# Optimization experiments

Measured on AMD Instinct MI355X. Metric: run time of the kernel, lower is better.

Reference implementation:

```python
import jax, jax.numpy as jnp
import numpy as np

BOUND = 10.0
EPS = 1e-06
MIN_SCALE = 1e-4


def _params_to_spline(raw_w, raw_h, raw_s, bound):
    # Standard Durkan et al. rational-quadratic spline parameterization.
    # raw_w/raw_h: (1, D, K); raw_s: (1, D, K+1)
    two_b = 2.0 * bound
    widths = jax.nn.softmax(raw_w[0], axis=-1) * two_b      # (D, K)
    heights = jax.nn.softmax(raw_h[0], axis=-1) * two_b     # (D, K)
    zero = jnp.zeros(widths.shape[:-1] + (1,), widths.dtype)
    xk = -bound + jnp.concatenate([zero, jnp.cumsum(widths, axis=-1)], axis=-1)   # (D, K+1)
    yk = -bound + jnp.concatenate([zero, jnp.cumsum(heights, axis=-1)], axis=-1)  # (D, K+1)
    slopes = jax.nn.softplus(raw_s[0])                       # (D, K+1)
    return xk, yk, widths, heights, slopes


def _rqs_forward(z, xk, yk, widths, heights, slopes, bound):
    # z: (B, D); per-dim knots xk/yk: (D, K+1); widths/heights: (D, K); slopes: (D, K+1)
    B, D = z.shape
    K = widths.shape[-1]
    zc = jnp.clip(z, -bound, bound)
    # per-dim binary search over knot positions
    idx = jax.vmap(lambda knots, col: jnp.searchsorted(knots, col, side='right'),
                   in_axes=(0, 1), out_axes=1)(xk, zc) - 1
    idx = jnp.clip(idx, 0, K - 1)                            # (B, D)
    di = jnp.arange(D)[None, :]
    xk_sel = xk[di, idx]
    w_sel = widths[di, idx]
    yk_sel = yk[di, idx]
    h_sel = heights[di, idx]
    d0 = slopes[di, idx]
    d1 = slopes[di, idx + 1]
    theta = (zc - xk_sel) / w_sel
    s = h_sel / w_sel
    t1m = theta * (1.0 - theta)
    den = s + (d0 + d1 - 2.0 * s) * t1m
    y_in = yk_sel + h_sel * (s * theta * theta + d0 * t1m) / den
    inside = (z > -bound) & (z < bound)
    return jnp.where(inside, y_in, z)


def setup_inputs() -> dict:
    key = jax.random.key(0)
    ks = jax.random.split(key, 7)
    B, D, K = 8192, 1024, 64
    return {
        'u': jax.random.uniform(ks[0], (B, D), dtype=jnp.float32),
        'tau': jax.random.normal(ks[1], (B, 1), dtype=jnp.float32),
        'log_scale': jax.random.normal(ks[2], (D,), dtype=jnp.float32) * 0.1,
        'bias': jax.random.normal(ks[3], (D,), dtype=jnp.float32) * 0.1,
        'raw_w': jax.random.normal(ks[4], (1, D, K), dtype=jnp.float32) * 0.5,
        'raw_h': jax.random.normal(ks[5], (1, D, K), dtype=jnp.float32) * 0.5,
        'raw_s': jax.random.normal(ks[6], (1, D, K + 1), dtype=jnp.float32) * 0.5,
    }


def reference(u, tau, log_scale, bias, raw_w, raw_h, raw_s):
    # logit input transform
    u_safe = jnp.clip(u, EPS, 1.0 - EPS)
    z = jnp.log(u_safe) - jnp.log1p(-u_safe)
    xk, yk, widths, heights, slopes = _params_to_spline(raw_w, raw_h, raw_s, BOUND)
    z = _rqs_forward(z, xk, yk, widths, heights, slopes, BOUND)
    scale = jax.nn.softplus(log_scale) + MIN_SCALE
    q = z * scale[None, :] + bias[None, :]
    return tau * q  # tau (B,1) broadcasts to (B,D)
```

## Files before the change

kernel.cpp:

```cpp
#include <hip/hip_runtime.h>
#include <math.h>

#define BOUNDF 10.0f
#define EPSF 1e-6f
#define MIN_SCALEF 1e-4f
#define DD 1024
#define KK 64
#define KP1 65

#define TD 32
#define TR 128

__global__ __launch_bounds__(64) void rqs_precompute(
    const float* __restrict__ raw_w, const float* __restrict__ raw_h,
    const float* __restrict__ raw_s, const float* __restrict__ log_scale,
    float* __restrict__ xk, float* __restrict__ yk,
    float* __restrict__ sl, float* __restrict__ scale)
{
    const int d = blockIdx.x;
    const int k = threadIdx.x;

    float ew = __expf(raw_w[d * KK + k]);
    float eh = __expf(raw_h[d * KK + k]);

    float sw = ew, sh = eh;
#pragma unroll
    for (int off = 1; off < 64; off <<= 1) {
        sw += __shfl_xor(sw, off, 64);
        sh += __shfl_xor(sh, off, 64);
    }
    float wk = ew * (2.0f * BOUNDF) / sw;
    float hk = eh * (2.0f * BOUNDF) / sh;

    float cw = wk, ch = hk;
#pragma unroll
    for (int off = 1; off < 64; off <<= 1) {
        float tw = __shfl_up(cw, off, 64);
        float th = __shfl_up(ch, off, 64);
        if (k >= off) { cw += tw; ch += th; }
    }
    xk[d * KP1 + k + 1] = -BOUNDF + cw;
    yk[d * KP1 + k + 1] = -BOUNDF + ch;

    float rs = raw_s[d * KP1 + k];
    sl[d * KP1 + k] = log1pf(__expf(rs));
    if (k == 0) {
        xk[d * KP1] = -BOUNDF;
        yk[d * KP1] = -BOUNDF;
        float rs2 = raw_s[d * KP1 + KK];
        sl[d * KP1 + KK] = log1pf(__expf(rs2));
        scale[d] = log1pf(__expf(log_scale[d])) + MIN_SCALEF;
    }
}

__global__ __launch_bounds__(256, 6) void rqs_main(
    const float* __restrict__ u, const float* __restrict__ tau,
    const float* __restrict__ bias,
    const float* __restrict__ xk_g, const float* __restrict__ yk_g,
    const float* __restrict__ sl_g, const float* __restrict__ scale_g,
    float* __restrict__ out)
{
    __shared__ float lxk[TD * KP1];
    __shared__ float lyk[TD * KP1];
    __shared__ float lsl[TD * KP1];

    const int bx = blockIdx.x;
    const int dchunk = bx & (DD / TD - 1);
    const int rchunk = bx >> 5;
    const int d0 = dchunk * TD;
    const int r0 = rchunk * TR;
    const int t = threadIdx.x;

    for (int i = t; i < TD * KP1; i += 256) {
        lxk[i] = xk_g[d0 * KP1 + i];
        lyk[i] = yk_g[d0 * KP1 + i];
        lsl[i] = sl_g[d0 * KP1 + i];
    }
    __syncthreads();

    const int g = t & 7;
    const int rlane = t >> 3;
    const int dl = g * 4;
    const int dg = d0 + dl;

    float sc[4], bi[4];
    float kreg[4][7];
#pragma unroll
    for (int j = 0; j < 4; ++j) {
        sc[j] = scale_g[dg + j];
        bi[j] = bias[dg + j];
        const int base = (dl + j) * KP1;
#pragma unroll
        for (int i = 0; i < 7; ++i) kreg[j][i] = lxk[base + 8 * (i + 1)];
    }

    int b = r0 + rlane;
    float4 uu = *(const float4*)(u + (size_t)b * DD + dg);
    float tb = tau[b];

#pragma unroll 1
    for (int it = 0; it < TR / 32; ++it) {
        const int bcur = b;
        const float4 ucur = uu;
        const float tcur = tb;
        if (it + 1 < TR / 32) {
            const int bn = bcur + 32;
            uu = *(const float4*)(u + (size_t)bn * DD + dg);
            tb = tau[bn];
            b = bn;
        }
        float ua[4] = {ucur.x, ucur.y, ucur.z, ucur.w};
        float res[4];
#pragma unroll
        for (int j = 0; j < 4; ++j) {
            float uv = fminf(fmaxf(ua[j], EPSF), 1.0f - EPSF);
            float z = __logf(uv * __builtin_amdgcn_rcpf(1.0f - uv));
            float zc = fminf(fmaxf(z, -BOUNDF), BOUNDF);
            const int base = (dl + j) * KP1;
            int lo = (zc >= kreg[j][3]) ? 32 : 0;
            float m16 = (lo & 32) ? kreg[j][5] : kreg[j][1];
            lo += (zc >= m16) ? 16 : 0;
            float a8 = (lo & 32) ? kreg[j][4] : kreg[j][0];
            float b8 = (lo & 32) ? kreg[j][6] : kreg[j][2];
            float m8 = (lo & 16) ? b8 : a8;
            lo += (zc >= m8) ? 8 : 0;
            lo += (lxk[base + lo + 4] <= zc) ? 4 : 0;
            lo += (lxk[base + lo + 2] <= zc) ? 2 : 0;
            lo += (lxk[base + lo + 1] <= zc) ? 1 : 0;
            float x0 = lxk[base + lo], x1 = lxk[base + lo + 1];
            float y0 = lyk[base + lo], y1 = lyk[base + lo + 1];
            float s0 = lsl[base + lo], s1 = lsl[base + lo + 1];
            float w = x1 - x0, h = y1 - y0;
            float invw = __builtin_amdgcn_rcpf(w);
            float th = (zc - x0) * invw;
            float sm = h * invw;
            float t1m = th * (1.0f - th);
            float den = fmaf(fmaf(-2.0f, sm, s0 + s1), t1m, sm);
            float num = h * fmaf(sm * th, th, s0 * t1m);
            float y = fmaf(num, __builtin_amdgcn_rcpf(den), y0);
            y = (z > -BOUNDF && z < BOUNDF) ? y : z;
            res[j] = tcur * fmaf(y, sc[j], bi[j]);
        }
        float4 ro = make_float4(res[0], res[1], res[2], res[3]);
        *(float4*)(out + (size_t)bcur * DD + dg) = ro;
    }
}

extern "C" void kernel_launch(void* const* d_in, const int* in_sizes, int n_in,
                              void* d_out, int out_size, void* d_ws, size_t ws_size,
                              hipStream_t stream)
{
    const float* u         = (const float*)d_in[0];
    const float* tau       = (const float*)d_in[1];
    const float* log_scale = (const float*)d_in[2];
    const float* bias      = (const float*)d_in[3];
    const float* raw_w     = (const float*)d_in[4];
    const float* raw_h     = (const float*)d_in[5];
    const float* raw_s     = (const float*)d_in[6];
    float* out = (float*)d_out;

    float* ws    = (float*)d_ws;
    float* xk    = ws;
    float* yk    = xk + DD * KP1;
    float* sl    = yk + DD * KP1;
    float* scale = sl + DD * KP1;

    const int B = in_sizes[0] / DD;

    rqs_precompute<<<DD, 64, 0, stream>>>(raw_w, raw_h, raw_s, log_scale,
                                          xk, yk, sl, scale);
    rqs_main<<<(DD / TD) * (B / TR), 256, 0, stream>>>(u, tau, bias,
                                                       xk, yk, sl, scale, out);
}
```

Baseline: 111.0 us.

## Fuse spline precompute into main kernel and use grid-accelerated bin lookup

Removes the separate precompute launch. Each block now builds its own spline tables (softmax, cumsum, softplus) for 16 dims in shared memory. The binary search is replaced by a 256-cell lookup grid that gives a starting bin, followed by a short linear advance. Per-bin x, y, inverse width and height are packed into a float4 so one LDS load fetches them. This cuts a kernel launch and several dependent LDS lookups per element, but every block now redundantly recomputes the parameters for its dims, and the tile shape changes to TD=16, TR=256.

```diff
diff --git a/kernel.cpp b/kernel.cpp
--- a/kernel.cpp
+++ b/kernel.cpp
@@ -8,106 +8,101 @@
 #define KK 64
 #define KP1 65
 
-#define TD 32
-#define TR 128
+#define TD 16
+#define NCELL 256
+#define TR 256
+#define ITER (TR / 64)
 
-__global__ __launch_bounds__(64) void rqs_precompute(
-    const float* __restrict__ raw_w, const float* __restrict__ raw_h,
-    const float* __restrict__ raw_s, const float* __restrict__ log_scale,
-    float* __restrict__ xk, float* __restrict__ yk,
-    float* __restrict__ sl, float* __restrict__ scale)
-{
-    const int d = blockIdx.x;
-    const int k = threadIdx.x;
-
-    float ew = __expf(raw_w[d * KK + k]);
-    float eh = __expf(raw_h[d * KK + k]);
-
-    float sw = ew, sh = eh;
-#pragma unroll
-    for (int off = 1; off < 64; off <<= 1) {
-        sw += __shfl_xor(sw, off, 64);
-        sh += __shfl_xor(sh, off, 64);
-    }
-    float wk = ew * (2.0f * BOUNDF) / sw;
-    float hk = eh * (2.0f * BOUNDF) / sh;
-
-    float cw = wk, ch = hk;
-#pragma unroll
-    for (int off = 1; off < 64; off <<= 1) {
-        float tw = __shfl_up(cw, off, 64);
-        float th = __shfl_up(ch, off, 64);
-        if (k >= off) { cw += tw; ch += th; }
-    }
-    xk[d * KP1 + k + 1] = -BOUNDF + cw;
-    yk[d * KP1 + k + 1] = -BOUNDF + ch;
-
-    float rs = raw_s[d * KP1 + k];
-    sl[d * KP1 + k] = log1pf(__expf(rs));
-    if (k == 0) {
-        xk[d * KP1] = -BOUNDF;
-        yk[d * KP1] = -BOUNDF;
-        float rs2 = raw_s[d * KP1 + KK];
-        sl[d * KP1 + KK] = log1pf(__expf(rs2));
-        scale[d] = log1pf(__expf(log_scale[d])) + MIN_SCALEF;
-    }
+__device__ __forceinline__ float softplus_f(float x) {
+    return fmaxf(x, 0.0f) + __logf(1.0f + __expf(-fabsf(x)));
 }
 
-__global__ __launch_bounds__(256, 6) void rqs_main(
+__global__ __launch_bounds__(256, 5) void rqs_fused(
     const float* __restrict__ u, const float* __restrict__ tau,
-    const float* __restrict__ bias,
-    const float* __restrict__ xk_g, const float* __restrict__ yk_g,
-    const float* __restrict__ sl_g, const float* __restrict__ scale_g,
-    float* __restrict__ out)
+    const float* __restrict__ log_scale, const float* __restrict__ bias,
+    const float* __restrict__ raw_w, const float* __restrict__ raw_h,
+    const float* __restrict__ raw_s, float* __restrict__ out)
 {
-    __shared__ float lxk[TD * KP1];
-    __shared__ float lyk[TD * KP1];
-    __shared__ float lsl[TD * KP1];
+    __shared__ float4 livt[TD * KK];
+    __shared__ float  lxk[TD * KP1];
+    __shared__ float  lsl[TD * KP1];
+    __shared__ unsigned char lgr[TD * NCELL];
 
     const int bx = blockIdx.x;
     const int dchunk = bx & (DD / TD - 1);
-    const int rchunk = bx >> 5;
+    const int rchunk = bx >> 6;
     const int d0 = dchunk * TD;
     const int r0 = rchunk * TR;
     const int t = threadIdx.x;
+    const int wv = t >> 6;
+    const int lane = t & 63;
 
-    for (int i = t; i < TD * KP1; i += 256) {
-        lxk[i] = xk_g[d0 * KP1 + i];
-        lyk[i] = yk_g[d0 * KP1 + i];
-        lsl[i] = sl_g[d0 * KP1 + i];
+    for (int jd = 0; jd < 4; ++jd) {
+        const int dl = wv * 4 + jd;
+        const int d = d0 + dl;
+        float ew = __expf(raw_w[d * KK + lane]);
+        float eh = __expf(raw_h[d * KK + lane]);
+        float sw = ew, sh = eh;
+#pragma unroll
+        for (int off = 1; off < 64; off <<= 1) {
+            sw += __shfl_xor(sw, off, 64);
+            sh += __shfl_xor(sh, off, 64);
+        }
+        float wk = ew * ((2.0f * BOUNDF) / sw);
+        float hk = eh * ((2.0f * BOUNDF) / sh);
+        float cw = wk, ch = hk;
+#pragma unroll
+        for (int off = 1; off < 64; off <<= 1) {
+            float aw = __shfl_up(cw, off, 64);
+            float ah = __shfl_up(ch, off, 64);
+            if (lane >= off) { cw += aw; ch += ah; }
+        }
+        float cwp = __shfl_up(cw, 1, 64); if (lane == 0) cwp = 0.0f;
+        float chp = __shfl_up(ch, 1, 64); if (lane == 0) chp = 0.0f;
+        float X  = -BOUNDF + cwp;
+        float Yv = -BOUNDF + chp;
+        float Xn = (lane == 63) ? BOUNDF : (-BOUNDF + cw);
+        float Yn = (lane == 63) ? BOUNDF : (-BOUNDF + ch);
+        float invw = 1.0f / (Xn - X);
+        livt[dl * KK + lane] = make_float4(X, Yv, invw, Yn - Yv);
+        lxk[dl * KP1 + lane] = X;
+        lsl[dl * KP1 + lane] = softplus_f(raw_s[d * KP1 + lane]);
+        if (lane == 63) {
+            lxk[dl * KP1 + 64] = BOUNDF;
+            lsl[dl * KP1 + 64] = softplus_f(raw_s[d * KP1 + 64]);
+        }
+        int c0 = (int)ceilf(cwp * (NCELL / (2.0f * BOUNDF)));
+        int c1 = (lane == 63) ? NCELL
+                              : (int)ceilf(cw * (NCELL / (2.0f * BOUNDF)));
+        c1 = min(c1, NCELL);
+        for (int c = c0; c < c1; ++c) lgr[dl * NCELL + c] = (unsigned char)lane;
     }
     __syncthreads();
 
-    const int g = t & 7;
-    const int rlane = t >> 3;
-    const int dl = g * 4;
-    const int dg = d0 + dl;
+    const int g4 = (t & 3) * 4;
+    const int rl = t >> 2;
+    const int dg = d0 + g4;
 
     float sc[4], bi[4];
-    float kreg[4][7];
 #pragma unroll
     for (int j = 0; j < 4; ++j) {
-        sc[j] = scale_g[dg + j];
+        sc[j] = softplus_f(log_scale[dg + j]) + MIN_SCALEF;
         bi[j] = bias[dg + j];
-        const int base = (dl + j) * KP1;
-#pragma unroll
-        for (int i = 0; i < 7; ++i) kreg[j][i] = lxk[base + 8 * (i + 1)];
     }
 
-    int b = r0 + rlane;
+    int b = r0 + rl;
     float4 uu = *(const float4*)(u + (size_t)b * DD + dg);
     float tb = tau[b];
 
 #pragma unroll 1
-    for (int it = 0; it < TR / 32; ++it) {
-        const int bcur = b;
+    for (int it = 0; it < ITER; ++it) {
         const float4 ucur = uu;
         const float tcur = tb;
-        if (it + 1 < TR / 32) {
-            const int bn = bcur + 32;
-            uu = *(const float4*)(u + (size_t)bn * DD + dg);
-            tb = tau[bn];
-            b = bn;
+        const int bcur = b;
+        if (it + 1 < ITER) {
+            b += 64;
+            uu = *(const float4*)(u + (size_t)b * DD + dg);
+            tb = tau[b];
         }
         float ua[4] = {ucur.x, ucur.y, ucur.z, ucur.w};
         float res[4];
@@ -115,34 +110,31 @@
         for (int j = 0; j < 4; ++j) {
             float uv = fminf(fmaxf(ua[j], EPSF), 1.0f - EPSF);
             float z = __logf(uv * __builtin_amdgcn_rcpf(1.0f - uv));
-            float zc = fminf(fmaxf(z, -BOUNDF), BOUNDF);
-            const int base = (dl + j) * KP1;
-            int lo = (zc >= kreg[j][3]) ? 32 : 0;
-            float m16 = (lo & 32) ? kreg[j][5] : kreg[j][1];
-            lo += (zc >= m16) ? 16 : 0;
-            float a8 = (lo & 32) ? kreg[j][4] : kreg[j][0];
-            float b8 = (lo & 32) ? kreg[j][6] : kreg[j][2];
-            float m8 = (lo & 16) ? b8 : a8;
-            lo += (zc >= m8) ? 8 : 0;
-            lo += (lxk[base + lo + 4] <= zc) ? 4 : 0;
-            lo += (lxk[base + lo + 2] <= zc) ? 2 : 0;
-            lo += (lxk[base + lo + 1] <= zc) ? 1 : 0;
-            float x0 = lxk[base + lo], x1 = lxk[base + lo + 1];
-            float y0 = lyk[base + lo], y1 = lyk[base + lo + 1];
-            float s0 = lsl[base + lo], s1 = lsl[base + lo + 1];
-            float w = x1 - x0, h = y1 - y0;
-            float invw = __builtin_amdgcn_rcpf(w);
-            float th = (zc - x0) * invw;
-            float sm = h * invw;
+            float zc = fminf(fmaxf(z, -BOUNDF), 9.9999990f);
+            const int bxk = (g4 + j) * KP1;
+            int cell = (int)fmaf(zc, NCELL / (2.0f * BOUNDF), 0.5f * NCELL);
+            int lo = (int)lgr[(g4 + j) * NCELL + cell];
+            float nx = lxk[bxk + lo + 1];
+            bool adv = (nx <= zc);
+            while (__any(adv)) {
+                lo += adv;
+                nx = lxk[bxk + lo + 1];
+                adv = adv && (nx <= zc);
+            }
+            float4 iv = livt[(g4 + j) * KK + lo];
+            float dd0 = lsl[bxk + lo];
+            float dd1 = lsl[bxk + lo + 1];
+            float th  = (zc - iv.x) * iv.z;
+            float s   = iv.w * iv.z;
             float t1m = th * (1.0f - th);
-            float den = fmaf(fmaf(-2.0f, sm, s0 + s1), t1m, sm);
-            float num = h * fmaf(sm * th, th, s0 * t1m);
-            float y = fmaf(num, __builtin_amdgcn_rcpf(den), y0);
-            y = (z > -BOUNDF && z < BOUNDF) ? y : z;
+            float den = fmaf(fmaf(-2.0f, s, dd0 + dd1), t1m, s);
+            float num = iv.w * fmaf(s * th, th, dd0 * t1m);
+            float y = fmaf(num, __builtin_amdgcn_rcpf(den), iv.y);
+            y = (fabsf(z) < BOUNDF) ? y : z;
             res[j] = tcur * fmaf(y, sc[j], bi[j]);
         }
-        float4 ro = make_float4(res[0], res[1], res[2], res[3]);
-        *(float4*)(out + (size_t)bcur * DD + dg) = ro;
+        *(float4*)(out + (size_t)bcur * DD + dg) =
+            make_float4(res[0], res[1], res[2], res[3]);
     }
 }
 
@@ -159,16 +151,7 @@
     const float* raw_s     = (const float*)d_in[6];
     float* out = (float*)d_out;
 
-    float* ws    = (float*)d_ws;
-    float* xk    = ws;
-    float* yk    = xk + DD * KP1;
-    float* sl    = yk + DD * KP1;
-    float* scale = sl + DD * KP1;
-
     const int B = in_sizes[0] / DD;
-
-    rqs_precompute<<<DD, 64, 0, stream>>>(raw_w, raw_h, raw_s, log_scale,
-                                          xk, yk, sl, scale);
-    rqs_main<<<(DD / TD) * (B / TR), 256, 0, stream>>>(u, tau, bias,
-                                                       xk, yk, sl, scale, out);
+    rqs_fused<<<(DD / TD) * (B / TR), 256, 0, stream>>>(
+        u, tau, log_scale, bias, raw_w, raw_h, raw_s, out);
 }
```

Measured after the change: 115.6 us. +4.2%, slower.
